# Performance work log

Hardware: AMD Instinct MI355X
Metric: run time of the kernel (lower is better)

The kernel has to match this reference:

```python
import jax, jax.numpy as jnp
import numpy as np

# init constants (match init_kwargs)
NGH, SUB_Q, SUB_D, POS_D, NEG_D, BORDER, SUB_D_NEG = 7, 8, 1, 2, 4, 16, 8
BATCH_STRIDE = 512.0  # hardcoded `b * 512` offset in the original cdist call


def _offsets():
    # faithful port of NghSampler.precompute_offsets
    rad = (NGH // SUB_D) * NGH
    pos, neg = [], []
    for j in range(-rad, rad + 1, SUB_D):
        for i in range(-rad, rad + 1, SUB_D):
            d2 = i * i + j * j
            if d2 <= POS_D ** 2:
                pos.append((i, j))
            elif NEG_D ** 2 <= d2 <= NGH ** 2:
                neg.append((i, j))
    return np.array(pos, np.int32).T, np.array(neg, np.int32).T  # [2,P],[2,Nn]


def _grid(step, B, H, W):
    # gen_grid with step > 0: regular grid inside the border, flattened
    xs = np.arange(BORDER, W - BORDER, step)
    ys = np.arange(BORDER, H - BORDER, step)
    H1, W1 = len(ys), len(xs)
    b = np.repeat(np.arange(B), H1 * W1)
    y = np.tile(np.repeat(ys, W1), B)
    x = np.tile(np.tile(xs, H1), B)
    return b, y, x, (B, H1, W1)


def setup_inputs() -> dict:
    key = jax.random.key(0)
    B, D, H, W = 2, 128, 512, 512
    k1, k2, k3, k4, k5 = jax.random.split(key, 5)
    pos_off, neg_off = _offsets()
    return {
        "feat1": jax.random.normal(k1, (B, D, H, W), jnp.float32),
        "feat2": jax.random.normal(k2, (B, D, H, W), jnp.float32),
        "conf1": jax.random.uniform(k3, (B, 1, H, W), jnp.float32),
        "conf2": jax.random.uniform(k4, (B, 1, H, W), jnp.float32),
        # dense flow: target (x, y) coords in image 2, a few out of bounds
        "aflow": jax.random.uniform(k5, (B, 2, H, W), jnp.float32, -10.0, W + 10.0),
        "pos_offsets": jnp.asarray(pos_off),
        "neg_offsets": jnp.asarray(neg_off),
    }


def reference(feat1, feat2, conf1, conf2, aflow, pos_offsets, neg_offsets):
    B, two, H, W = aflow.shape
    b1, y1, x1, shape = _grid(SUB_Q, B, H, W)      # n = B*H1*W1 query points

    f1 = feat1[b1, :, y1, x1]                      # [n, D]
    qconf = conf1[b1, 0, y1, x1].reshape(shape)    # (B, H1, W1)

    # (aflow + 0.5).long(): truncation toward zero, as torch .long()
    xy2 = jnp.transpose(aflow[b1, :, y1, x1] + 0.5).astype(jnp.int32)  # [2, n]
    mask = ((xy2[0] >= 0) & (xy2[1] >= 0) & (xy2[0] < W) & (xy2[1] < H)).reshape(shape)

    def clamp(xy):
        return jnp.stack([jnp.clip(xy[0], 0, W - 1), jnp.clip(xy[1], 0, H - 1)])

    # positive ring: gather feat2 at offset pixels -> [P, n, D], dot with f1
    xy2p = clamp(xy2[:, None, :] + pos_offsets[:, :, None])  # [2, P, n]
    pscores = jnp.einsum('nk,pnk->np', f1, feat2[b1, :, xy2p[1], xy2p[0]])
    # negative ring -> [Nn, n, D]
    xy2n = clamp(xy2[:, None, :] + neg_offsets[:, :, None])  # [2, Nn, n]
    nscores = jnp.einsum('nk,ink->ni', f1, feat2[b1, :, xy2n[1], xy2n[0]])

    # distractors: regular grid over image 2
    b3, y3, x3, _ = _grid(SUB_D_NEG, B, H, W)      # n3 points
    d3 = feat2[b3, :, y3, x3]                      # [n3, D]
    dscores = jnp.einsum('nk,ik->ni', f1, d3)      # [n, n3]

    # cdist with per-batch 512 offset (un-clamped xy2, as in the original)
    qx = xy2[0].astype(jnp.float32) + BATCH_STRIDE * b1
    qy = xy2[1].astype(jnp.float32) + BATCH_STRIDE * b1
    dx = x3.astype(np.float32) + BATCH_STRIDE * b3
    dy = y3.astype(np.float32) + BATCH_STRIDE * b3
    dis = jnp.sqrt((qx[:, None] - dx[None, :]) ** 2 + (qy[:, None] - dy[None, :]) ** 2)
    dscores = jnp.where(dis < NEG_D, 0.0, dscores)

    scores = jnp.concatenate([pscores, nscores, dscores], axis=1)
    n, P = pscores.shape
    gt = jnp.concatenate([jnp.ones((n, P), jnp.uint8),
                          jnp.zeros((n, scores.shape[1] - P), jnp.uint8)], axis=1)
    return scores, gt, mask, qconf
```

## Files before the change

### kernel.cpp

```cpp
#include <hip/hip_runtime.h>
#include <hip/hip_bf16.h>
#include <stdint.h>

#define B_ 2
#define D_ 128
#define H_ 512
#define W_ 512
#define G_ 60
#define NQ_ 7200
#define BORDER_ 16
#define STEP_ 8

typedef __attribute__((ext_vector_type(8))) short short8;
typedef __attribute__((ext_vector_type(4))) float f32x4;
typedef __attribute__((ext_vector_type(4))) uint32_t u32x4;

__device__ __forceinline__ float bf_lo(uint32_t u){ return __builtin_bit_cast(float, u << 16); }
__device__ __forceinline__ float bf_hi(uint32_t u){ return __builtin_bit_cast(float, u & 0xffff0000u); }

__device__ __forceinline__ uint32_t pack2bf(float lo, float hi){
  uint16_t l = __builtin_bit_cast(uint16_t, __float2bfloat16(lo));
  uint16_t h = __builtin_bit_cast(uint16_t, __float2bfloat16(hi));
  return (uint32_t)l | ((uint32_t)h << 16);
}

__global__ __launch_bounds__(256) void gtzero_k(f32x4* __restrict__ gt, size_t n4){
  size_t i = (size_t)blockIdx.x * 256 + threadIdx.x;
  size_t stride = (size_t)gridDim.x * 256;
  f32x4 z = {0.f, 0.f, 0.f, 0.f};
  for (; i < n4; i += stride)
    __builtin_nontemporal_store(z, gt + i);
}

__global__ __launch_bounds__(256) void transpose_k(const float* __restrict__ src,
                                                   __hip_bfloat16* __restrict__ dst){
  __shared__ uint32_t lds2[64][65];
  int b = blockIdx.z, y = blockIdx.y, x0 = blockIdx.x * 64;
  int tid = threadIdx.x;
  size_t plane = (size_t)H_ * W_;

  int xq = tid & 15;
  int eg = tid >> 4;
  size_t base_in = (((size_t)b * D_) * H_ + y) * W_ + x0 + 4 * xq;
  #pragma unroll
  for (int it = 0; it < 4; ++it){
    int e = eg + 16 * it;
    f32x4 lo = __builtin_nontemporal_load(
        reinterpret_cast<const f32x4*>(src + base_in + (size_t)(2 * e) * plane));
    f32x4 hi = __builtin_nontemporal_load(
        reinterpret_cast<const f32x4*>(src + base_in + (size_t)(2 * e + 1) * plane));
    lds2[e][4 * xq + 0] = pack2bf(lo[0], hi[0]);
    lds2[e][4 * xq + 1] = pack2bf(lo[1], hi[1]);
    lds2[e][4 * xq + 2] = pack2bf(lo[2], hi[2]);
    lds2[e][4 * xq + 3] = pack2bf(lo[3], hi[3]);
  }
  __syncthreads();

  int eq = tid & 15;
  int xb = tid >> 4;
  size_t pixbase = (((size_t)b * H_ + y) * W_ + x0);
  #pragma unroll
  for (int it = 0; it < 4; ++it){
    int x = xb + 16 * it;
    u32x4 v;
    v[0] = lds2[4 * eq + 0][x];
    v[1] = lds2[4 * eq + 1][x];
    v[2] = lds2[4 * eq + 2][x];
    v[3] = lds2[4 * eq + 3][x];
    *reinterpret_cast<u32x4*>(dst + (pixbase + x) * D_ + 8 * eq) = v;
  }
}

template<bool USE_T>
__global__ __launch_bounds__(128) void prep_k(
    const float* __restrict__ feat1, const float* __restrict__ feat2,
    const __hip_bfloat16* __restrict__ f2t,
    const float* __restrict__ conf1, const float* __restrict__ aflow,
    __hip_bfloat16* __restrict__ f1o, __hip_bfloat16* __restrict__ d3o,
    float2* __restrict__ qxy, float2* __restrict__ dxy,
    float* __restrict__ omask, float* __restrict__ oqconf)
{
  int n = blockIdx.x;
  int b = n / (G_ * G_); int r = n % (G_ * G_);
  int iy = r / G_, ix = r % G_;
  int y1 = BORDER_ + iy * STEP_, x1 = BORDER_ + ix * STEP_;
  int tid = threadIdx.x;
  size_t pix = ((size_t)b * H_ + y1) * W_ + x1;
  if (tid < 64){
    int d = tid * 2;
    size_t o = (((size_t)b * D_ + d) * H_ + y1) * W_ + x1;
    float lo = feat1[o];
    float hi = feat1[o + (size_t)H_ * W_];
    *reinterpret_cast<uint32_t*>(f1o + (size_t)n * D_ + d) = pack2bf(lo, hi);
    if (tid == 0){
      float ax = aflow[(((size_t)b * 2 + 0) * H_ + y1) * W_ + x1];
      float ay = aflow[(((size_t)b * 2 + 1) * H_ + y1) * W_ + x1];
      int x2 = (int)(ax + 0.5f);
      int y2 = (int)(ay + 0.5f);
      omask[n] = (x2 >= 0 && y2 >= 0 && x2 < W_ && y2 < H_) ? 1.0f : 0.0f;
      oqconf[n] = conf1[pix];
      float bs = 512.0f * (float)b;
      qxy[n] = make_float2((float)x2 + bs, (float)y2 + bs);
      dxy[n] = make_float2((float)x1 + bs, (float)y1 + bs);
    }
  } else {
    int d = (tid - 64) * 2;
    uint32_t u;
    if (USE_T){
      u = *reinterpret_cast<const uint32_t*>(f2t + pix * D_ + d);
    } else {
      size_t o = (((size_t)b * D_ + d) * H_ + y1) * W_ + x1;
      u = pack2bf(feat2[o], feat2[o + (size_t)H_ * W_]);
    }
    *reinterpret_cast<uint32_t*>(d3o + (size_t)n * D_ + d) = u;
  }
}

template<bool USE_T>
__global__ __launch_bounds__(256) void posneg_k(
    const __hip_bfloat16* __restrict__ f1o,
    const __hip_bfloat16* __restrict__ f2t,
    const float* __restrict__ feat2,
    const float* __restrict__ aflow,
    const int* __restrict__ pos, const int* __restrict__ neg,
    int P, int NN, float* __restrict__ out, int NCOL, size_t GTOFF)
{
  int n = blockIdx.x;
  int b = n / (G_ * G_); int r = n % (G_ * G_);
  int iy = r / G_, ix = r % G_;
  int y1 = BORDER_ + iy * STEP_, x1 = BORDER_ + ix * STEP_;
  int tid = threadIdx.x;
  int l16 = tid & 15, grp = tid >> 4;

  const uint4 av = *reinterpret_cast<const uint4*>(f1o + (size_t)n * D_ + l16 * 8);
  float a[8];
  a[0] = bf_lo(av.x); a[1] = bf_hi(av.x); a[2] = bf_lo(av.y); a[3] = bf_hi(av.y);
  a[4] = bf_lo(av.z); a[5] = bf_hi(av.z); a[6] = bf_lo(av.w); a[7] = bf_hi(av.w);

  float ax = aflow[(((size_t)b * 2 + 0) * H_ + y1) * W_ + x1];
  float ay = aflow[(((size_t)b * 2 + 1) * H_ + y1) * W_ + x1];
  int x2 = (int)(ax + 0.5f), y2 = (int)(ay + 0.5f);

  int NP = P + NN;
  for (int p0 = 0; p0 < NP; p0 += 16){
    int p = p0 + grp;
    float s = 0.0f;
    if (p < NP){
      int ox, oy;
      if (p < P){ ox = pos[p]; oy = pos[P + p]; }
      else      { ox = neg[p - P]; oy = neg[NN + p - P]; }
      int px = min(max(x2 + ox, 0), W_ - 1);
      int py = min(max(y2 + oy, 0), H_ - 1);
      if (USE_T){
        const uint4 v = *reinterpret_cast<const uint4*>(
            f2t + (((size_t)b * H_ + py) * W_ + px) * D_ + l16 * 8);
        s = a[0]*bf_lo(v.x) + a[1]*bf_hi(v.x) + a[2]*bf_lo(v.y) + a[3]*bf_hi(v.y)
          + a[4]*bf_lo(v.z) + a[5]*bf_hi(v.z) + a[6]*bf_lo(v.w) + a[7]*bf_hi(v.w);
      } else {
        size_t o = (((size_t)b * D_ + l16 * 8) * H_ + py) * W_ + px;
        #pragma unroll
        for (int j = 0; j < 8; ++j) s += a[j] * feat2[o + (size_t)j * H_ * W_];
      }
    }
    s += __shfl_xor(s, 1); s += __shfl_xor(s, 2);
    s += __shfl_xor(s, 4); s += __shfl_xor(s, 8);
    if (p < NP && l16 == 0){
      size_t idx = (size_t)n * NCOL + p;
      out[idx] = s;
      out[GTOFF + idx] = (p < P) ? 1.0f : 0.0f;
    }
  }
}

__global__ __launch_bounds__(256) void gemm_k(
    const __hip_bfloat16* __restrict__ f1o, const __hip_bfloat16* __restrict__ d3o,
    const float2* __restrict__ qxy, const float2* __restrict__ dxy,
    float* __restrict__ out, int NCOL, int CB)
{
  __shared__ float sT[32][97];
  int m0 = blockIdx.y * 96, n0 = blockIdx.x * 96;
  int tid = threadIdx.x;
  int lane = tid & 63, wid = tid >> 6;
  int wr = wid >> 1, wc = wid & 1;
  int r16 = lane & 15, kg = lane >> 4;

  f32x4 acc[3][3] = {};
  #pragma unroll
  for (int ks = 0; ks < 4; ++ks){
    int k0 = ks * 32 + kg * 8;
    short8 af[3], br[3];
    #pragma unroll
    for (int i = 0; i < 3; ++i){
      int m = m0 + wr * 48 + i * 16 + r16;
      af[i] = *reinterpret_cast<const short8*>(f1o + (size_t)m * D_ + k0);
      int nn = n0 + wc * 48 + i * 16 + r16;
      br[i] = *reinterpret_cast<const short8*>(d3o + (size_t)nn * D_ + k0);
    }
    #pragma unroll
    for (int j = 0; j < 3; ++j)
      #pragma unroll
      for (int i = 0; i < 3; ++i)
        acc[j][i] = __builtin_amdgcn_mfma_f32_16x16x32_bf16(br[j], af[i], acc[j][i], 0, 0, 0);
  }

  #pragma unroll
  for (int i = 0; i < 3; ++i){
    __syncthreads();
    #pragma unroll
    for (int j = 0; j < 3; ++j){
      f32x4 v = acc[j][i];
      int col = wc * 48 + j * 16 + kg * 4;
      #pragma unroll
      for (int t = 0; t < 4; ++t)
        sT[wr * 16 + r16][col + t] = v[t];
    }
    __syncthreads();
    #pragma unroll
    for (int k = 0; k < 8; ++k){
      int ri = wid * 8 + k;
      int m = m0 + (ri >> 4) * 48 + i * 16 + (ri & 15);
      float2 q = qxy[m];
      size_t ro = (size_t)m * NCOL + CB + n0;
      #pragma unroll
      for (int half = 0; half < 2; ++half){
        int c = half * 64 + lane;
        if (c < 96){
          float2 dc = dxy[n0 + c];
          float v = sT[ri][c];
          float ddx = q.x - dc.x, ddy = q.y - dc.y;
          out[ro + c] = (ddx * ddx + ddy * ddy < 16.0f) ? 0.0f : v;
        }
      }
    }
  }
}

extern "C" void kernel_launch(void* const* d_in, const int* in_sizes, int n_in,
                              void* d_out, int out_size, void* d_ws, size_t ws_size,
                              hipStream_t stream)
{
  const float* feat1 = (const float*)d_in[0];
  const float* feat2 = (const float*)d_in[1];
  const float* conf1 = (const float*)d_in[2];
  const float* aflow = (const float*)d_in[4];
  const int* pos = (const int*)d_in[5];
  const int* neg = (const int*)d_in[6];
  int P = in_sizes[5] / 2, NN = in_sizes[6] / 2;
  int NCOL = P + NN + NQ_;
  size_t GTOFF = (size_t)NQ_ * (size_t)NCOL;
  float* out = (float*)d_out;

  char* ws = (char*)d_ws;
  __hip_bfloat16* f1o = (__hip_bfloat16*)ws;
  __hip_bfloat16* d3o = (__hip_bfloat16*)(ws + 1843200);
  float2* qxy = (float2*)(ws + 3686400);
  float2* dxy = (float2*)(ws + 3744000);
  __hip_bfloat16* f2t = (__hip_bfloat16*)(ws + 3801600);
  size_t needT = 3801600ull + (size_t)B_ * H_ * W_ * D_ * 2;
  bool useT = ws_size >= needT;

  float* omask  = out + 2 * GTOFF;
  float* oqconf = omask + NQ_;

  gtzero_k<<<2048, 256, 0, stream>>>((f32x4*)(out + GTOFF), GTOFF / 4);

  if (useT){
    transpose_k<<<dim3(W_ / 64, H_, B_), 256, 0, stream>>>(feat2, f2t);
    prep_k<true><<<NQ_, 128, 0, stream>>>(feat1, feat2, f2t, conf1, aflow,
                                          f1o, d3o, qxy, dxy, omask, oqconf);
    posneg_k<true><<<NQ_, 256, 0, stream>>>(f1o, f2t, feat2, aflow, pos, neg,
                                            P, NN, out, NCOL, GTOFF);
  } else {
    prep_k<false><<<NQ_, 128, 0, stream>>>(feat1, feat2, f2t, conf1, aflow,
                                           f1o, d3o, qxy, dxy, omask, oqconf);
    posneg_k<false><<<NQ_, 256, 0, stream>>>(f1o, f2t, feat2, aflow, pos, neg,
                                             P, NN, out, NCOL, GTOFF);
  }
  gemm_k<<<dim3(NQ_ / 96, NQ_ / 96), 256, 0, stream>>>(f1o, d3o, qxy, dxy,
                                                       out, NCOL, P + NN);
}
```

Measured before the change: 299.7 us.

## Restructure distractor GEMM into row-strip blocks sweeping all columns

The distractor-score GEMM now gives each block a 16-row strip of queries and loops over all 7200 distractor columns in chunks of 256, keeping the query A-fragments in registers for the whole sweep. Output writes are realigned so each row segment starts on a 64-byte boundary, to make the strided row stores into the wide output matrix more contiguous. The cost is a much longer serial loop per block (450 blocks instead of 5625), fewer MFMAs per loaded B fragment, and B data re-read from global or L2 by every block.

```diff
diff --git a/kernel.cpp b/kernel.cpp
--- a/kernel.cpp
+++ b/kernel.cpp
@@ -177,61 +177,65 @@
     const float2* __restrict__ qxy, const float2* __restrict__ dxy,
     float* __restrict__ out, int NCOL, int CB)
 {
-  __shared__ float sT[32][97];
-  int m0 = blockIdx.y * 96, n0 = blockIdx.x * 96;
+  __shared__ float sT[16][264];
+  int m0 = blockIdx.x * 16;
   int tid = threadIdx.x;
   int lane = tid & 63, wid = tid >> 6;
-  int wr = wid >> 1, wc = wid & 1;
   int r16 = lane & 15, kg = lane >> 4;
-
-  f32x4 acc[3][3] = {};
+  int wbase = wid * 64;
+
+  short8 af[4];
   #pragma unroll
-  for (int ks = 0; ks < 4; ++ks){
-    int k0 = ks * 32 + kg * 8;
-    short8 af[3], br[3];
+  for (int ks = 0; ks < 4; ++ks)
+    af[ks] = *reinterpret_cast<const short8*>(
+        f1o + (size_t)(m0 + r16) * D_ + ks * 32 + kg * 8);
+
+  for (int cn0 = 0; cn0 < NQ_; cn0 += 256){
+    int nc = NQ_ - cn0; if (nc > 256) nc = 256;
+
+    f32x4 acc[4] = {};
     #pragma unroll
-    for (int i = 0; i < 3; ++i){
-      int m = m0 + wr * 48 + i * 16 + r16;
-      af[i] = *reinterpret_cast<const short8*>(f1o + (size_t)m * D_ + k0);
-      int nn = n0 + wc * 48 + i * 16 + r16;
-      br[i] = *reinterpret_cast<const short8*>(d3o + (size_t)nn * D_ + k0);
-    }
+    for (int j = 0; j < 4; ++j){
+      if (wbase + j * 16 < nc){
+        int nn = cn0 + wbase + j * 16 + r16;
+        #pragma unroll
+        for (int ks = 0; ks < 4; ++ks){
+          short8 br = *reinterpret_cast<const short8*>(
+              d3o + (size_t)nn * D_ + ks * 32 + kg * 8);
+          acc[j] = __builtin_amdgcn_mfma_f32_16x16x32_bf16(br, af[ks], acc[j], 0, 0, 0);
+        }
+      }
+    }
+
     #pragma unroll
-    for (int j = 0; j < 3; ++j)
-      #pragma unroll
-      for (int i = 0; i < 3; ++i)
-        acc[j][i] = __builtin_amdgcn_mfma_f32_16x16x32_bf16(br[j], af[i], acc[j][i], 0, 0, 0);
-  }
-
-  #pragma unroll
-  for (int i = 0; i < 3; ++i){
+    for (int j = 0; j < 4; ++j)
+      if (wbase + j * 16 < nc)
+        *reinterpret_cast<f32x4*>(&sT[r16][wbase + j * 16 + kg * 4]) = acc[j];
     __syncthreads();
+
     #pragma unroll
-    for (int j = 0; j < 3; ++j){
-      f32x4 v = acc[j][i];
-      int col = wc * 48 + j * 16 + kg * 4;
-      #pragma unroll
-      for (int t = 0; t < 4; ++t)
-        sT[wr * 16 + r16][col + t] = v[t];
+    for (int k = 0; k < 4; ++k){
+      int r = wid * 4 + k;
+      int m = m0 + r;
+      float2 q = qxy[m];
+      size_t S = (size_t)m * NCOL + CB + cn0;
+      int skip = (int)((16 - (S & 15)) & 15);
+      if (lane < skip && lane < nc){
+        int c = lane;
+        float2 dc = dxy[cn0 + c];
+        float ddx = q.x - dc.x, ddy = q.y - dc.y;
+        out[S + c] = (ddx * ddx + ddy * ddy < 16.0f) ? 0.0f : sT[r][c];
+      }
+      for (int b = 0; skip + b * 64 < nc; ++b){
+        int c = skip + b * 64 + lane;
+        if (c < nc){
+          float2 dc = dxy[cn0 + c];
+          float ddx = q.x - dc.x, ddy = q.y - dc.y;
+          out[S + c] = (ddx * ddx + ddy * ddy < 16.0f) ? 0.0f : sT[r][c];
+        }
+      }
     }
     __syncthreads();
-    #pragma unroll
-    for (int k = 0; k < 8; ++k){
-      int ri = wid * 8 + k;
-      int m = m0 + (ri >> 4) * 48 + i * 16 + (ri & 15);
-      float2 q = qxy[m];
-      size_t ro = (size_t)m * NCOL + CB + n0;
-      #pragma unroll
-      for (int half = 0; half < 2; ++half){
-        int c = half * 64 + lane;
-        if (c < 96){
-          float2 dc = dxy[n0 + c];
-          float v = sT[ri][c];
-          float ddx = q.x - dc.x, ddy = q.y - dc.y;
-          out[ro + c] = (ddx * ddx + ddy * ddy < 16.0f) ? 0.0f : v;
-        }
-      }
-    }
   }
 }
 
@@ -276,6 +280,5 @@
     posneg_k<false><<<NQ_, 256, 0, stream>>>(f1o, f2t, feat2, aflow, pos, neg,
                                              P, NN, out, NCOL, GTOFF);
   }
-  gemm_k<<<dim3(NQ_ / 96, NQ_ / 96), 256, 0, stream>>>(f1o, d3o, qxy, dxy,
-                                                       out, NCOL, P + NN);
-}
+  gemm_k<<<NQ_ / 16, 256, 0, stream>>>(f1o, d3o, qxy, dxy, out, NCOL, P + NN);
+}
```

Measured after the change: 386.3 us. 28.9% more time.
